# Optimization experiments

Measured on AMD Instinct MI355X. Metric: run time of the kernel, lower is better.

Reference implementation:

```python
import jax, jax.numpy as jnp
import numpy as np

N_NODES = 50000
N_EDGES = 800000
D = 64
NEG_SLOPE = 0.2  # PyG GATConv default


def gat_layer(x, W, a_src, a_dst, b, src, dst, n):
    """Single-head GATConv (PyG semantics, self-loops already in src/dst)."""
    h = x @ W                                   # [N, d_out]
    # attention logit per edge (j -> i): a_src.h_j + a_dst.h_i
    e = jax.nn.leaky_relu((h @ a_src)[src] + (h @ a_dst)[dst], NEG_SLOPE)  # [E]
    # segment softmax over incoming edges of each destination node
    m = jax.ops.segment_max(e, dst, num_segments=n)          # [N]
    p = jnp.exp(e - jax.lax.stop_gradient(m)[dst])           # [E]
    s = jax.ops.segment_sum(p, dst, num_segments=n)          # [N]
    alpha = p / s[dst]                                       # [E]
    out = jax.ops.segment_sum(alpha[:, None] * h[src], dst, num_segments=n)
    return out + b


def setup_inputs() -> dict:
    key = jax.random.key(0)
    ks = jax.random.split(key, 10)
    sc = 1.0 / np.sqrt(D)
    return {
        "embeds": jax.random.normal(ks[0], (N_NODES, D), jnp.float32),
        "edges": jax.random.randint(ks[1], (2, N_EDGES), 0, N_NODES, jnp.int64),
        "W1": jax.random.normal(ks[2], (D, D), jnp.float32) * sc,
        "a_src1": jax.random.normal(ks[3], (D,), jnp.float32) * sc,
        "a_dst1": jax.random.normal(ks[4], (D,), jnp.float32) * sc,
        "b1": jnp.zeros((D,), jnp.float32),
        "W2": jax.random.normal(ks[5], (D, D), jnp.float32) * sc,
        "a_src2": jax.random.normal(ks[6], (D,), jnp.float32) * sc,
        "a_dst2": jax.random.normal(ks[7], (D,), jnp.float32) * sc,
        "b2": jnp.zeros((D,), jnp.float32),
    }


def reference(embeds, edges, W1, a_src1, a_dst1, b1, W2, a_src2, a_dst2, b2):
    n = embeds.shape[0]
    # PyG GATConv adds self-loops by default
    loop = jnp.arange(n, dtype=edges.dtype)
    src = jnp.concatenate([edges[0], loop])
    dst = jnp.concatenate([edges[1], loop])
    h = jax.nn.relu(gat_layer(embeds, W1, a_src1, a_dst1, b1, src, dst, n))
    return gat_layer(h, W2, a_src2, a_dst2, b2, src, dst, n)
```

## Files before the change

### kernel.cpp

```cpp
#include <hip/hip_runtime.h>

#define D 64
#define CAP 48
#define NCB 256
#define SCAPS 40
#define RCAP 512
#define PBLK 256
#define NSUB 8
#define CPAD 8

typedef __attribute__((ext_vector_type(8))) __bf16 bf16x8;
typedef __attribute__((ext_vector_type(4))) float f32x4;

__device__ __forceinline__ unsigned short f2b(float f) {
    unsigned int u = __float_as_uint(f);
    return (unsigned short)((u + 0x7fffu + ((u >> 16) & 1u)) >> 16);
}


__global__ __launch_bounds__(256) void zero_kernel(int* __restrict__ p, int n) {
    int idx = blockIdx.x * 256 + threadIdx.x;
    if (idx < n) p[idx] = 0;
}


__global__ __launch_bounds__(256) void partition_kernel(
    const int* __restrict__ edges, int E, int npcb,
    int* __restrict__ cnt, unsigned int* __restrict__ bl)
{
    __shared__ unsigned int stage[NCB * SCAPS];
    __shared__ int cnt_l[NCB];
    __shared__ int gbase[NCB];

    int blk = blockIdx.x;
    int g = blk & (NSUB - 1);
    int t = threadIdx.x;

    cnt_l[t] = 0;
    __syncthreads();

    int chunk = (E + PBLK - 1) / PBLK;
    int e0 = blk * chunk;
    int e1 = e0 + chunk; if (e1 > E) e1 = E;

    for (int e = e0 + t; e < e1; e += 256) {
        int s = edges[e];
        int d = edges[E + e];
        int cb = d / npcb;
        int dl = d - cb * npcb;
        int pos = atomicAdd(&cnt_l[cb], 1);
        if (pos < SCAPS)
            stage[cb * SCAPS + pos] = ((unsigned int)dl << 16) | (unsigned int)s;
    }
    __syncthreads();

    int c = cnt_l[t]; if (c > SCAPS) c = SCAPS;
    gbase[t] = atomicAdd(&cnt[(g * NCB + t) * CPAD], c);
    __syncthreads();

    int gb = gbase[t];
    size_t rbase = (size_t)(g * NCB + t) * RCAP;
    for (int j = 0; j < c; ++j) {
        int idx = gb + j;
        if (idx < RCAP) bl[rbase + idx] = stage[t * SCAPS + j];
    }
}


template <bool SRC_F32>
__device__ __forceinline__ void gemm_tile(
    const void* __restrict__ xin, const float* __restrict__ W,
    const float* __restrict__ a_src, const float* __restrict__ a_dst,
    unsigned short* __restrict__ hb, float* __restrict__ hs,
    float* __restrict__ hd, int N, int tile)
{
    int t = threadIdx.x;
    int wave = t >> 6, lane = t & 63, lr = lane & 15, lg = lane >> 4;
    int row0 = tile * 64 + wave * 16;

    bf16x8 bfr[4][2];
    #pragma unroll
    for (int c = 0; c < 4; ++c)
        #pragma unroll
        for (int kk = 0; kk < 2; ++kk) {
            union { unsigned short u[8]; bf16x8 v; } tb;
            #pragma unroll
            for (int e = 0; e < 8; ++e)
                tb.u[e] = f2b(W[(kk * 32 + lg * 8 + e) * 64 + c * 16 + lr]);
            bfr[c][kk] = tb.v;
        }

    int arow = row0 + lr; if (arow >= N) arow = N - 1;
    bf16x8 afr[2];
    if constexpr (SRC_F32) {
        const float* xf = (const float*)xin;
        #pragma unroll
        for (int kk = 0; kk < 2; ++kk) {
            const float4* pr = (const float4*)(xf + (size_t)arow * D + kk * 32 + lg * 8);
            float4 v0 = pr[0], v1 = pr[1];
            union { unsigned short u[8]; bf16x8 v; } ta;
            ta.u[0]=f2b(v0.x); ta.u[1]=f2b(v0.y); ta.u[2]=f2b(v0.z); ta.u[3]=f2b(v0.w);
            ta.u[4]=f2b(v1.x); ta.u[5]=f2b(v1.y); ta.u[6]=f2b(v1.z); ta.u[7]=f2b(v1.w);
            afr[kk] = ta.v;
        }
    } else {
        const unsigned short* xb = (const unsigned short*)xin;
        #pragma unroll
        for (int kk = 0; kk < 2; ++kk) {
            union { uint4 r; bf16x8 v; } ta;
            ta.r = *(const uint4*)(xb + (size_t)arow * D + kk * 32 + lg * 8);
            afr[kk] = ta.v;
        }
    }

    f32x4 acc[4];
    #pragma unroll
    for (int c = 0; c < 4; ++c) acc[c] = (f32x4){0.f, 0.f, 0.f, 0.f};
    #pragma unroll
    for (int kk = 0; kk < 2; ++kk)
        #pragma unroll
        for (int c = 0; c < 4; ++c)
            acc[c] = __builtin_amdgcn_mfma_f32_16x16x32_bf16(afr[kk], bfr[c][kk],
                                                             acc[c], 0, 0, 0);

    float asv[4], adv[4];
    #pragma unroll
    for (int c = 0; c < 4; ++c) { asv[c] = a_src[c*16+lr]; adv[c] = a_dst[c*16+lr]; }

    #pragma unroll
    for (int r = 0; r < 4; ++r) {
        int row = row0 + lg * 4 + r;
        float vs = 0.f, vd = 0.f;
        #pragma unroll
        for (int c = 0; c < 4; ++c) {
            float hv = acc[c][r];
            if (row < N) hb[(size_t)row * D + c * 16 + lr] = f2b(hv);
            vs = fmaf(hv, asv[c], vs);
            vd = fmaf(hv, adv[c], vd);
        }
        #pragma unroll
        for (int off = 8; off; off >>= 1) {
            vs += __shfl_xor(vs, off);
            vd += __shfl_xor(vd, off);
        }
        if (lr == 0 && row < N) { hs[row] = vs; hd[row] = vd; }
    }
}


__global__ __launch_bounds__(256) void build_gemm1_kernel(
    const unsigned int* __restrict__ bl, const int* __restrict__ cnt,
    int* __restrict__ deg, unsigned short* __restrict__ csr, int npcb,
    const float* __restrict__ embeds, const float* __restrict__ W1,
    const float* __restrict__ as1, const float* __restrict__ ad1,
    unsigned short* __restrict__ hb, float* __restrict__ hs,
    float* __restrict__ hd, int N)
{
    int blk = blockIdx.x;
    if (blk >= NCB) {
        gemm_tile<true>(embeds, W1, as1, ad1, hb, hs, hd, N, blk - NCB);
        return;
    }

    __shared__ int deg_l[256];
    __shared__ unsigned short csr_l[196 * CAP];

    int cb = blk;
    int t = threadIdx.x;
    deg_l[t] = 0;
    __syncthreads();

    #pragma unroll
    for (int g = 0; g < NSUB; ++g) {
        int reg = g * NCB + cb;
        int c = cnt[reg * CPAD]; if (c > RCAP) c = RCAP;
        size_t rbase = (size_t)reg * RCAP;
        for (int k = t; k < c; k += 256) {
            unsigned int u = bl[rbase + k];
            int dl = u >> 16;
            int pos = atomicAdd(&deg_l[dl], 1);
            if (pos < CAP) csr_l[dl * CAP + pos] = (unsigned short)(u & 0xFFFF);
        }
    }
    __syncthreads();

    int n0 = cb * npcb;
    int nn = N - n0; if (nn > npcb) nn = npcb;
    if (nn <= 0) return;

    if (t < nn) deg[n0 + t] = deg_l[t];
    int tot = nn * CAP;
    for (int k = t; k < tot; k += 256)
        csr[(size_t)n0 * CAP + k] = csr_l[k];
}

__global__ __launch_bounds__(256) void gemm2_kernel(
    const unsigned short* __restrict__ x1b, const float* __restrict__ W2,
    const float* __restrict__ as2, const float* __restrict__ ad2,
    unsigned short* __restrict__ hb, float* __restrict__ hs,
    float* __restrict__ hd, int N)
{
    gemm_tile<false>(x1b, W2, as2, ad2, hb, hs, hd, N, blockIdx.x);
}


template <bool RELU>
__global__ __launch_bounds__(256) void gather_kernel(
    const unsigned short* __restrict__ hb,
    const float* __restrict__ hs, const float* __restrict__ hd,
    const int* __restrict__ deg, const unsigned short* __restrict__ csr,
    const float* __restrict__ bias, void* __restrict__ outv, int N)
{
    int t = threadIdx.x;
    int wave = t >> 6;
    int lane = t & 63;
    int i0 = (blockIdx.x * 4 + wave) * 2;
    if (i0 >= N) return;

    int half = lane >> 5;
    int hl = lane & 31;
    int g2 = (lane >> 4) & 1;
    int f = lane & 15;

    int i = i0 + half;
    bool valid = (i < N);
    int iw = valid ? i : i0;

    int start = iw * CAP;
    int cnt_i = 0;
    if (valid) {
        cnt_i = deg[iw]; if (cnt_i > CAP) cnt_i = CAP;
        cnt_i += 1;
    }
    float hdv = hd[iw];

    int cother = __shfl_xor(cnt_i, 32);
    int cmax = cnt_i > cother ? cnt_i : cother;

    float s = 0.f;
    float o0 = 0.f, o1 = 0.f, o2 = 0.f, o3 = 0.f;

    for (int base = 0; base < cmax; base += 32) {
        int v = base + hl;
        int myj = 0; float p = 0.f;
        if (v < cnt_i) {
            myj = (v == 0) ? iw : (int)csr[start + v - 1];
            float l = hs[myj] + hdv;
            l = (l > 0.f) ? l : 0.2f * l;
            p = __expf(l);
        }

        float cs = p;
        #pragma unroll
        for (int off = 16; off; off >>= 1) cs += __shfl_xor(cs, off);
        s += cs;

        int remw = cmax - base; if (remw > 32) remw = 32;
        int iters = (remw + 1) >> 1;
        #pragma unroll 4
        for (int it = 0; it < iters; ++it) {
            int e = it * 2 + g2;
            int sl = half * 32 + e;
            int j = __shfl(myj, sl);
            float pp = __shfl(p, sl);
            uint2 hv = *(const uint2*)(hb + (size_t)j * 64 + f * 4);
            o0 = fmaf(pp, __uint_as_float(hv.x << 16), o0);
            o1 = fmaf(pp, __uint_as_float(hv.x & 0xffff0000u), o1);
            o2 = fmaf(pp, __uint_as_float(hv.y << 16), o2);
            o3 = fmaf(pp, __uint_as_float(hv.y & 0xffff0000u), o3);
        }
    }

    o0 += __shfl_xor(o0, 16);
    o1 += __shfl_xor(o1, 16);
    o2 += __shfl_xor(o2, 16);
    o3 += __shfl_xor(o3, 16);

    if (g2 == 0 && valid) {
        float4 bv = ((const float4*)bias)[f];
        float inv = 1.f / s;
        float r0 = fmaf(o0, inv, bv.x);
        float r1 = fmaf(o1, inv, bv.y);
        float r2 = fmaf(o2, inv, bv.z);
        float r3 = fmaf(o3, inv, bv.w);
        if (RELU) {
            r0 = fmaxf(r0, 0.f); r1 = fmaxf(r1, 0.f);
            r2 = fmaxf(r2, 0.f); r3 = fmaxf(r3, 0.f);
            uint2 pk;
            pk.x = ((unsigned int)f2b(r1) << 16) | f2b(r0);
            pk.y = ((unsigned int)f2b(r3) << 16) | f2b(r2);
            ((uint2*)outv)[(size_t)i * 16 + f] = pk;
        } else {
            float4 r; r.x = r0; r.y = r1; r.z = r2; r.w = r3;
            ((float4*)outv)[(size_t)i * 16 + f] = r;
        }
    }
}


extern "C" void kernel_launch(void* const* d_in, const int* in_sizes, int n_in,
                              void* d_out, int out_size, void* d_ws, size_t ws_size,
                              hipStream_t stream)
{
    const float* embeds = (const float*)d_in[0];
    const int*   edges  = (const int*)d_in[1];
    const float* W1  = (const float*)d_in[2];
    const float* as1 = (const float*)d_in[3];
    const float* ad1 = (const float*)d_in[4];
    const float* b1  = (const float*)d_in[5];
    const float* W2  = (const float*)d_in[6];
    const float* as2 = (const float*)d_in[7];
    const float* ad2 = (const float*)d_in[8];
    const float* b2  = (const float*)d_in[9];

    int N = in_sizes[0] / D;
    int E = in_sizes[1] / 2;
    int npcb = (N + NCB - 1) / NCB;

    char* ws = (char*)d_ws;
    unsigned short* hb  = (unsigned short*)ws;  ws += (size_t)N * D * 2;
    unsigned short* x1b = (unsigned short*)ws;  ws += (size_t)N * D * 2;
    float* hs = (float*)ws;          ws += (size_t)N * 4;
    float* hd = (float*)ws;          ws += (size_t)N * 4;
    int* cnt  = (int*)ws;            ws += (size_t)NSUB * NCB * CPAD * 4;
    unsigned int* bl = (unsigned int*)ws;  ws += (size_t)NSUB * NCB * RCAP * 4;
    int* deg  = (int*)ws;            ws += (size_t)N * 4;
    unsigned short* csr = (unsigned short*)ws;  ws += (size_t)N * CAP * 2;

    const int tb = 256;
    int nbM = (N + 63) / 64;
    int nbG = (N + 7) / 8;
    int nZ = NSUB * NCB * CPAD;

    zero_kernel<<<(nZ + tb - 1) / tb, tb, 0, stream>>>(cnt, nZ);
    partition_kernel<<<PBLK, tb, 0, stream>>>(edges, E, npcb, cnt, bl);
    build_gemm1_kernel<<<NCB + nbM, tb, 0, stream>>>(
        bl, cnt, deg, csr, npcb, embeds, W1, as1, ad1, hb, hs, hd, N);
    gather_kernel<true><<<nbG, tb, 0, stream>>>(hb, hs, hd, deg, csr, b1, x1b, N);
    gemm2_kernel<<<nbM, tb, 0, stream>>>(x1b, W2, as2, ad2, hb, hs, hd, N);
    gather_kernel<false><<<nbG, tb, 0, stream>>>(hb, hs, hd, deg, csr, b2,
                                                 (float*)d_out, N);
}
```

Measured before the change: 99.53 us.

## Fuse layer-1 gather with layer-2 GEMM and drop atomic partition counters

The partition step now writes per-block, per-bucket counts and edge slots to fixed positions instead of atomically appending into shared sub-buckets. This removes the zero kernel and the global atomics. The build step reads one slot per thread, 256 slots per bucket, each looped serially. The layer-1 gather is fused with the layer-2 GEMM: relu outputs are staged in LDS as bf16 and fed straight to MFMA, which avoids a global round trip and a launch. The fused kernel has only 782 blocks, each handling 64 nodes serially per wave, which may reduce gather parallelism. Per-thread serial loops in the build step may be unbalanced.

Result: slower. 104.6 us (+5.0%).

```diff
diff --git a/kernel.cpp b/kernel.cpp
--- a/kernel.cpp
+++ b/kernel.cpp
@@ -4,10 +4,7 @@
 #define CAP 48
 #define NCB 256
 #define SCAPS 40
-#define RCAP 512
 #define PBLK 256
-#define NSUB 8
-#define CPAD 8
 
 typedef __attribute__((ext_vector_type(8))) __bf16 bf16x8;
 typedef __attribute__((ext_vector_type(4))) float f32x4;
@@ -18,22 +15,14 @@
 }
 
 
-__global__ __launch_bounds__(256) void zero_kernel(int* __restrict__ p, int n) {
-    int idx = blockIdx.x * 256 + threadIdx.x;
-    if (idx < n) p[idx] = 0;
-}
-
-
 __global__ __launch_bounds__(256) void partition_kernel(
     const int* __restrict__ edges, int E, int npcb,
-    int* __restrict__ cnt, unsigned int* __restrict__ bl)
+    int* __restrict__ cnt2, unsigned int* __restrict__ bl)
 {
     __shared__ unsigned int stage[NCB * SCAPS];
     __shared__ int cnt_l[NCB];
-    __shared__ int gbase[NCB];
 
     int blk = blockIdx.x;
-    int g = blk & (NSUB - 1);
     int t = threadIdx.x;
 
     cnt_l[t] = 0;
@@ -55,15 +44,10 @@
     __syncthreads();
 
     int c = cnt_l[t]; if (c > SCAPS) c = SCAPS;
-    gbase[t] = atomicAdd(&cnt[(g * NCB + t) * CPAD], c);
-    __syncthreads();
-
-    int gb = gbase[t];
-    size_t rbase = (size_t)(g * NCB + t) * RCAP;
-    for (int j = 0; j < c; ++j) {
-        int idx = gb + j;
-        if (idx < RCAP) bl[rbase + idx] = stage[t * SCAPS + j];
-    }
+    cnt2[blk * NCB + t] = c;
+    size_t rbase = ((size_t)blk * NCB + t) * SCAPS;
+    for (int j = 0; j < c; ++j)
+        bl[rbase + j] = stage[t * SCAPS + j];
 }
 
 
@@ -149,7 +133,7 @@
 
 
 __global__ __launch_bounds__(256) void build_gemm1_kernel(
-    const unsigned int* __restrict__ bl, const int* __restrict__ cnt,
+    const unsigned int* __restrict__ bl, const int* __restrict__ cnt2,
     int* __restrict__ deg, unsigned short* __restrict__ csr, int npcb,
     const float* __restrict__ embeds, const float* __restrict__ W1,
     const float* __restrict__ as1, const float* __restrict__ ad1,
@@ -170,17 +154,13 @@
     deg_l[t] = 0;
     __syncthreads();
 
-    #pragma unroll
-    for (int g = 0; g < NSUB; ++g) {
-        int reg = g * NCB + cb;
-        int c = cnt[reg * CPAD]; if (c > RCAP) c = RCAP;
-        size_t rbase = (size_t)reg * RCAP;
-        for (int k = t; k < c; k += 256) {
-            unsigned int u = bl[rbase + k];
-            int dl = u >> 16;
-            int pos = atomicAdd(&deg_l[dl], 1);
-            if (pos < CAP) csr_l[dl * CAP + pos] = (unsigned short)(u & 0xFFFF);
-        }
+    int c = cnt2[t * NCB + cb];
+    size_t rbase = ((size_t)t * NCB + cb) * SCAPS;
+    for (int k = 0; k < c; ++k) {
+        unsigned int u = bl[rbase + k];
+        int dl = u >> 16;
+        int pos = atomicAdd(&deg_l[dl], 1);
+        if (pos < CAP) csr_l[dl * CAP + pos] = (unsigned short)(u & 0xFFFF);
     }
     __syncthreads();
 
@@ -194,13 +174,152 @@
         csr[(size_t)n0 * CAP + k] = csr_l[k];
 }
 
-__global__ __launch_bounds__(256) void gemm2_kernel(
-    const unsigned short* __restrict__ x1b, const float* __restrict__ W2,
+
+__global__ __launch_bounds__(256) void gather1_gemm2_kernel(
+    const unsigned short* __restrict__ hb1,
+    const float* __restrict__ hs1, const float* __restrict__ hd1,
+    const int* __restrict__ deg, const unsigned short* __restrict__ csr,
+    const float* __restrict__ b1, const float* __restrict__ W2,
     const float* __restrict__ as2, const float* __restrict__ ad2,
-    unsigned short* __restrict__ hb, float* __restrict__ hs,
-    float* __restrict__ hd, int N)
-{
-    gemm_tile<false>(x1b, W2, as2, ad2, hb, hs, hd, N, blockIdx.x);
+    unsigned short* __restrict__ hb2, float* __restrict__ hs2,
+    float* __restrict__ hd2, int N)
+{
+    __shared__ unsigned short x1_l[64 * 72];
+
+    int t = threadIdx.x;
+    int w = t >> 6, lane = t & 63;
+    int half = lane >> 5;
+    int hl = lane & 31;
+    int g2 = (lane >> 4) & 1;
+    int f = lane & 15;
+
+    int nodeBase = blockIdx.x * 64 + w * 16;
+    float4 bv = ((const float4*)b1)[f];
+
+    for (int pp = 0; pp < 8; ++pp) {
+        int i0 = nodeBase + pp * 2;
+        if (i0 >= N) break;
+
+        int i = i0 + half;
+        bool valid = (i < N);
+        int iw = valid ? i : i0;
+
+        int start = iw * CAP;
+        int cnt_i = 0;
+        if (valid) {
+            cnt_i = deg[iw]; if (cnt_i > CAP) cnt_i = CAP;
+            cnt_i += 1;
+        }
+        float hdv = hd1[iw];
+
+        int cother = __shfl_xor(cnt_i, 32);
+        int cmax = cnt_i > cother ? cnt_i : cother;
+
+        float s = 0.f, o0 = 0.f, o1 = 0.f, o2 = 0.f, o3 = 0.f;
+
+        for (int base = 0; base < cmax; base += 32) {
+            int v = base + hl;
+            int myj = 0; float p = 0.f;
+            if (v < cnt_i) {
+                myj = (v == 0) ? iw : (int)csr[start + v - 1];
+                float l = hs1[myj] + hdv;
+                l = (l > 0.f) ? l : 0.2f * l;
+                p = __expf(l);
+            }
+            float cs = p;
+            #pragma unroll
+            for (int off = 16; off; off >>= 1) cs += __shfl_xor(cs, off);
+            s += cs;
+
+            int remw = cmax - base; if (remw > 32) remw = 32;
+            int iters = (remw + 1) >> 1;
+            #pragma unroll 4
+            for (int it = 0; it < iters; ++it) {
+                int e = it * 2 + g2;
+                int sl = half * 32 + e;
+                int j = __shfl(myj, sl);
+                float pq = __shfl(p, sl);
+                uint2 hv = *(const uint2*)(hb1 + (size_t)j * 64 + f * 4);
+                o0 = fmaf(pq, __uint_as_float(hv.x << 16), o0);
+                o1 = fmaf(pq, __uint_as_float(hv.x & 0xffff0000u), o1);
+                o2 = fmaf(pq, __uint_as_float(hv.y << 16), o2);
+                o3 = fmaf(pq, __uint_as_float(hv.y & 0xffff0000u), o3);
+            }
+        }
+        o0 += __shfl_xor(o0, 16);
+        o1 += __shfl_xor(o1, 16);
+        o2 += __shfl_xor(o2, 16);
+        o3 += __shfl_xor(o3, 16);
+
+        if (g2 == 0) {
+            float inv = valid ? (1.f / s) : 0.f;
+            float r0 = fmaxf(fmaf(o0, inv, bv.x), 0.f);
+            float r1 = fmaxf(fmaf(o1, inv, bv.y), 0.f);
+            float r2 = fmaxf(fmaf(o2, inv, bv.z), 0.f);
+            float r3 = fmaxf(fmaf(o3, inv, bv.w), 0.f);
+            uint2 pk;
+            pk.x = ((unsigned int)f2b(r1) << 16) | f2b(r0);
+            pk.y = ((unsigned int)f2b(r3) << 16) | f2b(r2);
+            int lrow = w * 16 + pp * 2 + half;
+            *(uint2*)(&x1_l[lrow * 72 + f * 4]) = pk;
+        }
+    }
+    __syncthreads();
+
+    int lr = lane & 15, lg = lane >> 4;
+
+    bf16x8 bfr[4][2];
+    #pragma unroll
+    for (int c = 0; c < 4; ++c)
+        #pragma unroll
+        for (int kk = 0; kk < 2; ++kk) {
+            union { unsigned short u[8]; bf16x8 v; } tb;
+            #pragma unroll
+            for (int e = 0; e < 8; ++e)
+                tb.u[e] = f2b(W2[(kk * 32 + lg * 8 + e) * 64 + c * 16 + lr]);
+            bfr[c][kk] = tb.v;
+        }
+
+    bf16x8 afr[2];
+    #pragma unroll
+    for (int kk = 0; kk < 2; ++kk) {
+        union { uint4 r; bf16x8 v; } ta;
+        ta.r = *(const uint4*)(&x1_l[(w * 16 + lr) * 72 + kk * 32 + lg * 8]);
+        afr[kk] = ta.v;
+    }
+
+    f32x4 acc[4];
+    #pragma unroll
+    for (int c = 0; c < 4; ++c) acc[c] = (f32x4){0.f, 0.f, 0.f, 0.f};
+    #pragma unroll
+    for (int kk = 0; kk < 2; ++kk)
+        #pragma unroll
+        for (int c = 0; c < 4; ++c)
+            acc[c] = __builtin_amdgcn_mfma_f32_16x16x32_bf16(afr[kk], bfr[c][kk],
+                                                             acc[c], 0, 0, 0);
+
+    float asv[4], adv[4];
+    #pragma unroll
+    for (int c = 0; c < 4; ++c) { asv[c] = as2[c*16+lr]; adv[c] = ad2[c*16+lr]; }
+
+    #pragma unroll
+    for (int r = 0; r < 4; ++r) {
+        int row = nodeBase + lg * 4 + r;
+        float vs = 0.f, vd = 0.f;
+        #pragma unroll
+        for (int c = 0; c < 4; ++c) {
+            float hv = acc[c][r];
+            if (row < N) hb2[(size_t)row * D + c * 16 + lr] = f2b(hv);
+            vs = fmaf(hv, asv[c], vs);
+            vd = fmaf(hv, adv[c], vd);
+        }
+        #pragma unroll
+        for (int off = 8; off; off >>= 1) {
+            vs += __shfl_xor(vs, off);
+            vd += __shfl_xor(vd, off);
+        }
+        if (lr == 0 && row < N) { hs2[row] = vs; hd2[row] = vd; }
+    }
 }
 
 
@@ -318,26 +437,27 @@
     int npcb = (N + NCB - 1) / NCB;
 
     char* ws = (char*)d_ws;
-    unsigned short* hb  = (unsigned short*)ws;  ws += (size_t)N * D * 2;
-    unsigned short* x1b = (unsigned short*)ws;  ws += (size_t)N * D * 2;
-    float* hs = (float*)ws;          ws += (size_t)N * 4;
-    float* hd = (float*)ws;          ws += (size_t)N * 4;
-    int* cnt  = (int*)ws;            ws += (size_t)NSUB * NCB * CPAD * 4;
-    unsigned int* bl = (unsigned int*)ws;  ws += (size_t)NSUB * NCB * RCAP * 4;
+    unsigned short* hb1 = (unsigned short*)ws;  ws += (size_t)N * D * 2;
+    unsigned short* hb2 = (unsigned short*)ws;  ws += (size_t)N * D * 2;
+    float* hs1 = (float*)ws;         ws += (size_t)N * 4;
+    float* hd1 = (float*)ws;         ws += (size_t)N * 4;
+    float* hs2 = (float*)ws;         ws += (size_t)N * 4;
+    float* hd2 = (float*)ws;         ws += (size_t)N * 4;
+    int* cnt2 = (int*)ws;            ws += (size_t)PBLK * NCB * 4;
+    unsigned int* bl = (unsigned int*)ws;  ws += (size_t)PBLK * NCB * SCAPS * 4;
     int* deg  = (int*)ws;            ws += (size_t)N * 4;
     unsigned short* csr = (unsigned short*)ws;  ws += (size_t)N * CAP * 2;
 
     const int tb = 256;
     int nbM = (N + 63) / 64;
+    int nbF = (N + 63) / 64;
     int nbG = (N + 7) / 8;
-    int nZ = NSUB * NCB * CPAD;
-
-    zero_kernel<<<(nZ + tb - 1) / tb, tb, 0, stream>>>(cnt, nZ);
-    partition_kernel<<<PBLK, tb, 0, stream>>>(edges, E, npcb, cnt, bl);
+
+    partition_kernel<<<PBLK, tb, 0, stream>>>(edges, E, npcb, cnt2, bl);
     build_gemm1_kernel<<<NCB + nbM, tb, 0, stream>>>(
-        bl, cnt, deg, csr, npcb, embeds, W1, as1, ad1, hb, hs, hd, N);
-    gather_kernel<true><<<nbG, tb, 0, stream>>>(hb, hs, hd, deg, csr, b1, x1b, N);
-    gemm2_kernel<<<nbM, tb, 0, stream>>>(x1b, W2, as2, ad2, hb, hs, hd, N);
-    gather_kernel<false><<<nbG, tb, 0, stream>>>(hb, hs, hd, deg, csr, b2,
+        bl, cnt2, deg, csr, npcb, embeds, W1, as1, ad1, hb1, hs1, hd1, N);
+    gather1_gemm2_kernel<<<nbF, tb, 0, stream>>>(
+        hb1, hs1, hd1, deg, csr, b1, W2, as2, ad2, hb2, hs2, hd2, N);
+    gather_kernel<false><<<nbG, tb, 0, stream>>>(hb2, hs2, hd2, deg, csr, b2,
                                                  (float*)d_out, N);
 }
```

## Replace atomic global bucket counters with per-block private slots, drop zero kernel

Applied to the files above, without the earlier changes.

The partition kernel now writes each block's per-bucket count and staged edges into a private slot indexed by (block, bucket), so it no longer needs global atomics. That removes the separate zeroing kernel launch. The build kernel has each thread read one partition block's slot for its bucket and insert those edges into shared memory. The cost is that each build thread walks its own slot serially, so the global reads become less coalesced, and the bucket workspace grows.

New measurement: 93.92 us. -5.6%, faster.

```diff
diff --git a/kernel.cpp b/kernel.cpp
--- a/kernel.cpp
+++ b/kernel.cpp
@@ -4,10 +4,7 @@
 #define CAP 48
 #define NCB 256
 #define SCAPS 40
-#define RCAP 512
 #define PBLK 256
-#define NSUB 8
-#define CPAD 8
 
 typedef __attribute__((ext_vector_type(8))) __bf16 bf16x8;
 typedef __attribute__((ext_vector_type(4))) float f32x4;
@@ -18,22 +15,14 @@
 }
 
 
-__global__ __launch_bounds__(256) void zero_kernel(int* __restrict__ p, int n) {
-    int idx = blockIdx.x * 256 + threadIdx.x;
-    if (idx < n) p[idx] = 0;
-}
-
-
 __global__ __launch_bounds__(256) void partition_kernel(
     const int* __restrict__ edges, int E, int npcb,
-    int* __restrict__ cnt, unsigned int* __restrict__ bl)
+    int* __restrict__ cnt2, unsigned int* __restrict__ bl)
 {
     __shared__ unsigned int stage[NCB * SCAPS];
     __shared__ int cnt_l[NCB];
-    __shared__ int gbase[NCB];
 
     int blk = blockIdx.x;
-    int g = blk & (NSUB - 1);
     int t = threadIdx.x;
 
     cnt_l[t] = 0;
@@ -55,15 +44,10 @@
     __syncthreads();
 
     int c = cnt_l[t]; if (c > SCAPS) c = SCAPS;
-    gbase[t] = atomicAdd(&cnt[(g * NCB + t) * CPAD], c);
-    __syncthreads();
-
-    int gb = gbase[t];
-    size_t rbase = (size_t)(g * NCB + t) * RCAP;
-    for (int j = 0; j < c; ++j) {
-        int idx = gb + j;
-        if (idx < RCAP) bl[rbase + idx] = stage[t * SCAPS + j];
-    }
+    cnt2[blk * NCB + t] = c;
+    size_t rbase = ((size_t)blk * NCB + t) * SCAPS;
+    for (int j = 0; j < c; ++j)
+        bl[rbase + j] = stage[t * SCAPS + j];
 }
 
 
@@ -149,7 +133,7 @@
 
 
 __global__ __launch_bounds__(256) void build_gemm1_kernel(
-    const unsigned int* __restrict__ bl, const int* __restrict__ cnt,
+    const unsigned int* __restrict__ bl, const int* __restrict__ cnt2,
     int* __restrict__ deg, unsigned short* __restrict__ csr, int npcb,
     const float* __restrict__ embeds, const float* __restrict__ W1,
     const float* __restrict__ as1, const float* __restrict__ ad1,
@@ -170,17 +154,13 @@
     deg_l[t] = 0;
     __syncthreads();
 
-    #pragma unroll
-    for (int g = 0; g < NSUB; ++g) {
-        int reg = g * NCB + cb;
-        int c = cnt[reg * CPAD]; if (c > RCAP) c = RCAP;
-        size_t rbase = (size_t)reg * RCAP;
-        for (int k = t; k < c; k += 256) {
-            unsigned int u = bl[rbase + k];
-            int dl = u >> 16;
-            int pos = atomicAdd(&deg_l[dl], 1);
-            if (pos < CAP) csr_l[dl * CAP + pos] = (unsigned short)(u & 0xFFFF);
-        }
+    int c = cnt2[t * NCB + cb];
+    size_t rbase = ((size_t)t * NCB + cb) * SCAPS;
+    for (int k = 0; k < c; ++k) {
+        unsigned int u = bl[rbase + k];
+        int dl = u >> 16;
+        int pos = atomicAdd(&deg_l[dl], 1);
+        if (pos < CAP) csr_l[dl * CAP + pos] = (unsigned short)(u & 0xFFFF);
     }
     __syncthreads();
 
@@ -322,20 +302,18 @@
     unsigned short* x1b = (unsigned short*)ws;  ws += (size_t)N * D * 2;
     float* hs = (float*)ws;          ws += (size_t)N * 4;
     float* hd = (float*)ws;          ws += (size_t)N * 4;
-    int* cnt  = (int*)ws;            ws += (size_t)NSUB * NCB * CPAD * 4;
-    unsigned int* bl = (unsigned int*)ws;  ws += (size_t)NSUB * NCB * RCAP * 4;
+    int* cnt2 = (int*)ws;            ws += (size_t)PBLK * NCB * 4;
+    unsigned int* bl = (unsigned int*)ws;  ws += (size_t)PBLK * NCB * SCAPS * 4;
     int* deg  = (int*)ws;            ws += (size_t)N * 4;
     unsigned short* csr = (unsigned short*)ws;  ws += (size_t)N * CAP * 2;
 
     const int tb = 256;
     int nbM = (N + 63) / 64;
     int nbG = (N + 7) / 8;
-    int nZ = NSUB * NCB * CPAD;
-
-    zero_kernel<<<(nZ + tb - 1) / tb, tb, 0, stream>>>(cnt, nZ);
-    partition_kernel<<<PBLK, tb, 0, stream>>>(edges, E, npcb, cnt, bl);
+
+    partition_kernel<<<PBLK, tb, 0, stream>>>(edges, E, npcb, cnt2, bl);
     build_gemm1_kernel<<<NCB + nbM, tb, 0, stream>>>(
-        bl, cnt, deg, csr, npcb, embeds, W1, as1, ad1, hb, hs, hd, N);
+        bl, cnt2, deg, csr, npcb, embeds, W1, as1, ad1, hb, hs, hd, N);
     gather_kernel<true><<<nbG, tb, 0, stream>>>(hb, hs, hd, deg, csr, b1, x1b, N);
     gemm2_kernel<<<nbM, tb, 0, stream>>>(x1b, W2, as2, ad2, hb, hs, hd, N);
     gather_kernel<false><<<nbG, tb, 0, stream>>>(hb, hs, hd, deg, csr, b2,
```
